# Performance work log

Hardware: AMD Instinct MI355X
Metric: run time of the kernel (lower is better)

The kernel has to match this reference:

```python
import jax, jax.numpy as jnp
import numpy as np

B, T, C, D = 8, 4096, 1024, 128  # batch, seq (=block_size), dim_embd, head_features

def setup_inputs() -> dict:
    key = jax.random.key(0)
    k1, k2, k3, k4 = jax.random.split(key, 4)
    s = 0.02
    return {
        "x": jax.random.normal(k1, (B, T, C), dtype=jnp.float32),
        "wq": jax.random.normal(k2, (C, D), dtype=jnp.float32) * s,
        "wk": jax.random.normal(k3, (C, D), dtype=jnp.float32) * s,
        "wv": jax.random.normal(k4, (C, D), dtype=jnp.float32) * s,
    }

def reference(x, wq, wk, wv):
    # q,k,v: [B,T,D]
    q = jnp.einsum('btc,cd->btd', x, wq)
    k = jnp.einsum('btc,cd->btd', x, wk)
    v = jnp.einsum('btc,cd->btd', x, wv)
    scale = k.shape[-1] ** -0.5
    wei = jnp.einsum('bqd,bkd->bqk', q, k) * scale  # [B,T,T]
    causal = jnp.tril(jnp.ones((T, T), dtype=bool))
    wei = jnp.where(causal, wei, -jnp.inf)
    attn = jax.nn.softmax(wei, axis=-1)  # dropout p=0.0 -> identity
    out = jnp.einsum('bqk,bkd->bqd', attn, v)  # [B,T,D]
    return out
```

## Files before the change

### kernel.cpp

```cpp
#include <hip/hip_runtime.h>

#define TT 4096
#define CC 1024
#define DD 128

typedef __attribute__((ext_vector_type(8))) short s16x8;
typedef __attribute__((ext_vector_type(4))) short s16x4;
typedef __attribute__((ext_vector_type(8))) __bf16 bf16x8;
typedef __attribute__((ext_vector_type(4))) float f32x4;

__device__ __forceinline__ short f2bf(float f) {
    union { float f; unsigned u; } v; v.f = f;
    unsigned r = v.u + 0x7fffu + ((v.u >> 16) & 1u);
    return (short)(r >> 16);
}

__device__ __forceinline__ unsigned cvt_pk(float lo, float hi) {
    unsigned r;
    asm("v_cvt_pk_bf16_f32 %0, %1, %2" : "=v"(r) : "v"(lo), "v"(hi));
    return r;
}

__device__ __forceinline__ f32x4 mfma16(s16x8 a, s16x8 b, f32x4 c) {
    return __builtin_amdgcn_mfma_f32_16x16x32_bf16(
        __builtin_bit_cast(bf16x8, a), __builtin_bit_cast(bf16x8, b), c, 0, 0, 0);
}

__device__ __forceinline__ void gload_lds16(const short* g, short* l) {
    __builtin_amdgcn_global_load_lds(
        (const __attribute__((address_space(1))) void*)g,
        (__attribute__((address_space(3))) void*)l, 16, 0, 0);
}

__global__ void wt_kernel(const float* __restrict__ wq, const float* __restrict__ wk,
                          const float* __restrict__ wv, short* __restrict__ wT) {
    int idx = blockIdx.x * 256 + threadIdx.x;
    int d = idx & 127;
    int c = (idx >> 7) & 1023;
    int wsel = idx >> 17;
    const float* w = (wsel == 0) ? wq : (wsel == 1) ? wk : wv;
    float v = w[(size_t)c * DD + d];
    if (wsel == 0) v *= 0.08838834764831845f;
    wT[(size_t)wsel * DD * CC + (size_t)d * CC + c] = f2bf(v);
}

__global__ __launch_bounds__(512)
void qkv_kernel(const float* __restrict__ x, const short* __restrict__ wT,
                short* __restrict__ qo, short* __restrict__ ko, short* __restrict__ vTo) {
    __shared__ short lw[2][384 * 64];
    const int mt = blockIdx.x;
    const int tid = threadIdx.x, lane = tid & 63, wid = tid >> 6;
    const int l15 = lane & 15, g = lane >> 4;
    const int wm = wid >> 1, wn = wid & 1;
    const int arow = mt * 128 + wm * 32 + l15;
    const float* xr0 = x + (size_t)arow * CC + g * 8;
    const float* xr1 = xr0 + (size_t)16 * CC;

    const f32x4 fz = {0.f, 0.f, 0.f, 0.f};
    f32x4 acc[2][12];
#pragma unroll
    for (int mr = 0; mr < 2; mr++)
#pragma unroll
        for (int nr = 0; nr < 12; nr++) acc[mr][nr] = fz;

    const int swr = wid * 48;
    const short* wsrc = wT + (size_t)(swr + (lane >> 3)) * CC + (lane & 7) * 8;

    float4 pa[2][2][2];
#define LOADA(kc) do { \
    _Pragma("unroll") for (int mr_ = 0; mr_ < 2; mr_++) \
    _Pragma("unroll") for (int ks_ = 0; ks_ < 2; ks_++) { \
        const float* p_ = (mr_ ? xr1 : xr0) + (kc) * 64 + ks_ * 32; \
        pa[mr_][ks_][0] = *(const float4*)p_; \
        pa[mr_][ks_][1] = *(const float4*)(p_ + 4); } \
} while (0)
#define STAGEW(kc, buf) do { \
    _Pragma("unroll") for (int j_ = 0; j_ < 6; j_++) \
        gload_lds16(wsrc + (size_t)(j_ * 8) * CC + (kc) * 64, &lw[buf][(swr + j_ * 8) * 64]); \
} while (0)

    LOADA(0);
    STAGEW(0, 0);
    asm volatile("s_waitcnt vmcnt(0)" ::: "memory");
    __builtin_amdgcn_s_barrier();
    int cur = 0;

    for (int kc = 0; kc < 16; kc++) {
        s16x8 af[2][2];
#pragma unroll
        for (int mr = 0; mr < 2; mr++)
#pragma unroll
            for (int ks = 0; ks < 2; ks++) {
                union { unsigned u[4]; s16x8 v; } cv;
                cv.u[0] = cvt_pk(pa[mr][ks][0].x, pa[mr][ks][0].y);
                cv.u[1] = cvt_pk(pa[mr][ks][0].z, pa[mr][ks][0].w);
                cv.u[2] = cvt_pk(pa[mr][ks][1].x, pa[mr][ks][1].y);
                cv.u[3] = cvt_pk(pa[mr][ks][1].z, pa[mr][ks][1].w);
                af[mr][ks] = cv.v;
            }
        if (kc < 15) { LOADA(kc + 1); STAGEW(kc + 1, cur ^ 1); }
        __builtin_amdgcn_s_setprio(1);
#pragma unroll
        for (int ks = 0; ks < 2; ks++)
#pragma unroll
            for (int nr = 0; nr < 12; nr++) {
                const s16x8 bfg = *(const s16x8*)
                    &lw[cur][(wn * 192 + nr * 16 + l15) * 64 + ks * 32 + g * 8];
                acc[0][nr] = mfma16(af[0][ks], bfg, acc[0][nr]);
                acc[1][nr] = mfma16(af[1][ks], bfg, acc[1][nr]);
            }
        __builtin_amdgcn_s_setprio(0);
        asm volatile("s_waitcnt vmcnt(0) lgkmcnt(0)" ::: "memory");
        __builtin_amdgcn_s_barrier();
        cur ^= 1;
    }

    const int bidx = mt >> 5;
    const int tb = (mt & 31) * 128 + wm * 32;
#pragma unroll
    for (int mr = 0; mr < 2; mr++)
#pragma unroll
        for (int nr = 0; nr < 12; nr++) {
            const int n = wn * 192 + nr * 16 + l15;
            if (n < 256) {
                short* dst; int d;
                if (n < 128) { dst = qo; d = n; } else { dst = ko; d = n - 128; }
#pragma unroll
                for (int i = 0; i < 4; i++) {
                    int t = tb + mr * 16 + g * 4 + i;
                    dst[((size_t)bidx * TT + t) * DD + d] = f2bf(acc[mr][nr][i]);
                }
            } else {
                const int d = n - 256;
                const int t = tb + mr * 16 + g * 4;
                uint2 u;
                u.x = cvt_pk(acc[mr][nr][0], acc[mr][nr][1]);
                u.y = cvt_pk(acc[mr][nr][2], acc[mr][nr][3]);
                *(uint2*)(vTo + ((size_t)bidx * DD + d) * TT + t) = u;
            }
        }
}

__device__ __forceinline__ void attn_stage(const short* kT, const short* vT, int kv0,
                                           short* lkb, short* lvb, int wid, int lane) {
#pragma unroll
    for (int j = 0; j < 4; j++) {
        int rbk = wid * 16 + j * 4;
        int rk = rbk + (lane >> 4);
        int ck = (lane & 15) ^ (rk & 7);
        gload_lds16(kT + (size_t)(kv0 + rk) * DD + ck * 8, lkb + rbk * 128);
        int rbv = wid * 32 + j * 8;
        int dv = rbv + (lane >> 3);
        int cv = (lane & 7) ^ (dv & 7);
        gload_lds16(vT + (size_t)dv * TT + kv0 + cv * 8, lvb + rbv * 64);
    }
}

__global__ __launch_bounds__(256)
void attn_kernel(const short* __restrict__ qb, const short* __restrict__ kb,
                 const short* __restrict__ vb, float* __restrict__ out,
                 float* __restrict__ opart, float2* __restrict__ mlpart) {
    const int qt = blockIdx.x;
    const int c  = blockIdx.y;
    const int b  = blockIdx.z;
    const int t0 = c * 16;
    if (t0 > qt) return;
    const int t1 = (t0 + 16 < qt + 1) ? t0 + 16 : qt + 1;
    const int nc = (qt >> 4) + 1;

    __shared__ short lk[2][64 * 128];
    __shared__ short lv[2][128 * 64];
    __shared__ short lp[4][1024];
    const int tid = threadIdx.x, lane = tid & 63, wid = tid >> 6;
    const int l15 = lane & 15, g = lane >> 4;
    const int wq0 = qt * 64 + wid * 16;
    const short* kT = kb + (size_t)b * TT * DD;
    const short* vT = vb + (size_t)b * DD * TT;
    char* lpw = (char*)&lp[wid][0];
    const f32x4 fz = {0.f, 0.f, 0.f, 0.f};

    s16x8 qf[4];
    {
        const short* qp = qb + ((size_t)b * TT + wq0 + l15) * DD + g * 8;
#pragma unroll
        for (int ks = 0; ks < 4; ks++) qf[ks] = *(const s16x8*)(qp + ks * 32);
    }
    f32x4 o[8];
#pragma unroll
    for (int n = 0; n < 8; n++) o[n] = fz;
    float rmax = -1e30f, rsum = 0.f;

    attn_stage(kT, vT, t0 * 64, lk[0], lv[0], wid, lane);
    asm volatile("s_waitcnt vmcnt(0)" ::: "memory");
    __builtin_amdgcn_s_barrier();
    int cur = 0;

    for (int t = t0; t < t1; t++) {
        if (t + 1 < t1) attn_stage(kT, vT, (t + 1) * 64, lk[cur ^ 1], lv[cur ^ 1], wid, lane);
        const int kv0 = t * 64;
        const char* lkc = (const char*)&lk[cur][0];
        const char* lvc = (const char*)&lv[cur][0];

        f32x4 s[4];
        __builtin_amdgcn_s_setprio(1);
#pragma unroll
        for (int sub = 0; sub < 4; sub++) {
            f32x4 a = fz;
#pragma unroll
            for (int ks = 0; ks < 4; ks++) {
                int row = sub * 16 + l15;
                int byte = (row * 256 + ks * 64 + g * 16) ^ ((row & 7) << 4);
                s16x8 kf = *(const s16x8*)(lkc + byte);
                a = mfma16(kf, qf[ks], a);
            }
            s[sub] = a;
        }
        __builtin_amdgcn_s_setprio(0);
        if (t == qt) {
#pragma unroll
            for (int sub = 0; sub < 4; sub++)
#pragma unroll
                for (int i = 0; i < 4; i++) {
                    int k = kv0 + sub * 16 + 4 * g + i;
                    if (k > wq0 + l15) s[sub][i] = -1e30f;
                }
        }
        float m0 = s[0][0];
#pragma unroll
        for (int sub = 0; sub < 4; sub++)
#pragma unroll
            for (int i = 0; i < 4; i++) m0 = fmaxf(m0, s[sub][i]);
        m0 = fmaxf(m0, __shfl_xor(m0, 16));
        m0 = fmaxf(m0, __shfl_xor(m0, 32));
        float mnew = fmaxf(rmax, m0);
        float scal = __expf(rmax - mnew);
        rmax = mnew;
        float ls = 0.f;
#pragma unroll
        for (int sub = 0; sub < 4; sub++)
#pragma unroll
            for (int i = 0; i < 4; i++) {
                float pv = __expf(s[sub][i] - mnew);
                s[sub][i] = pv;
                ls += pv;
            }
        ls += __shfl_xor(ls, 16);
        ls += __shfl_xor(ls, 32);
        rsum = rsum * scal + ls;
#pragma unroll
        for (int sub = 0; sub < 4; sub++) {
            uint2 w01;
            w01.x = cvt_pk(s[sub][0], s[sub][1]);
            w01.y = cvt_pk(s[sub][2], s[sub][3]);
            int byte = (l15 * 128 + sub * 32 + g * 8) ^ ((l15 & 7) << 4);
            *(uint2*)(lpw + byte) = w01;
        }
#pragma unroll
        for (int n = 0; n < 8; n++)
#pragma unroll
            for (int i = 0; i < 4; i++) o[n][i] *= scal;
        __builtin_amdgcn_s_setprio(1);
#pragma unroll
        for (int ks2 = 0; ks2 < 2; ks2++) {
            int pbyte = (l15 * 128 + ks2 * 64 + g * 16) ^ ((l15 & 7) << 4);
            s16x8 pf = *(const s16x8*)(lpw + pbyte);
#pragma unroll
            for (int n = 0; n < 8; n++) {
                int vrow = n * 16 + l15;
                int vbyte = (vrow * 128 + ks2 * 64 + g * 16) ^ ((vrow & 7) << 4);
                s16x8 vf = *(const s16x8*)(lvc + vbyte);
                o[n] = mfma16(vf, pf, o[n]);
            }
        }
        __builtin_amdgcn_s_setprio(0);
        asm volatile("s_waitcnt vmcnt(0) lgkmcnt(0)" ::: "memory");
        __builtin_amdgcn_s_barrier();
        cur ^= 1;
    }

    const int r = wid * 16 + l15;
    if (nc == 1) {
        float inv = 1.0f / rsum;
        float* orow = out + ((size_t)b * TT + qt * 64 + r) * DD;
#pragma unroll
        for (int n = 0; n < 8; n++) {
            float4 w;
            w.x = o[n][0] * inv; w.y = o[n][1] * inv;
            w.z = o[n][2] * inv; w.w = o[n][3] * inv;
            *(float4*)(orow + n * 16 + 4 * g) = w;
        }
    } else {
        const size_t pb = ((size_t)b * 48 + (qt - 16)) * 4 + c;
        float* prow = opart + pb * (64 * 128) + (size_t)r * 128;
#pragma unroll
        for (int n = 0; n < 8; n++) {
            float4 w;
            w.x = o[n][0]; w.y = o[n][1]; w.z = o[n][2]; w.w = o[n][3];
            *(float4*)(prow + n * 16 + 4 * g) = w;
        }
        if (g == 0) {
            float2 s2; s2.x = rmax; s2.y = rsum;
            mlpart[pb * 64 + r] = s2;
        }
    }
}

__global__ __launch_bounds__(256)
void comb_kernel(const float* __restrict__ opart, const float2* __restrict__ mlpart,
                 float* __restrict__ out) {
    const int qtm = blockIdx.x;
    const int b = blockIdx.y;
    const int qt = 16 + qtm;
    const int nc = (qt >> 4) + 1;
    const int tid = threadIdx.x;
    const int row = tid >> 2, quad = tid & 3;
    const size_t base = ((size_t)b * 48 + qtm) * 4;

    float M = -3e38f;
    for (int cc = 0; cc < nc; cc++)
        M = fmaxf(M, mlpart[(base + cc) * 64 + row].x);

    float acc[32];
#pragma unroll
    for (int k = 0; k < 32; k++) acc[k] = 0.f;
    float L = 0.f;
    for (int cc = 0; cc < nc; cc++) {
        float2 s = mlpart[(base + cc) * 64 + row];
        float wgt = __expf(s.x - M);
        L += wgt * s.y;
        const float* src = opart + (base + cc) * (64 * 128) + (size_t)row * 128 + quad * 32;
#pragma unroll
        for (int k = 0; k < 8; k++) {
            float4 v = *(const float4*)(src + k * 4);
            acc[k * 4 + 0] += wgt * v.x;
            acc[k * 4 + 1] += wgt * v.y;
            acc[k * 4 + 2] += wgt * v.z;
            acc[k * 4 + 3] += wgt * v.w;
        }
    }
    float inv = 1.0f / L;
    float* dst = out + ((size_t)b * TT + qt * 64 + row) * DD + quad * 32;
#pragma unroll
    for (int k = 0; k < 8; k++) {
        float4 w;
        w.x = acc[k * 4 + 0] * inv; w.y = acc[k * 4 + 1] * inv;
        w.z = acc[k * 4 + 2] * inv; w.w = acc[k * 4 + 3] * inv;
        *(float4*)(dst + k * 4) = w;
    }
}

extern "C" void kernel_launch(void* const* d_in, const int* in_sizes, int n_in,
                              void* d_out, int out_size, void* d_ws, size_t ws_size,
                              hipStream_t stream) {
    const float* x  = (const float*)d_in[0];
    const float* wq = (const float*)d_in[1];
    const float* wk = (const float*)d_in[2];
    const float* wv = (const float*)d_in[3];
    float* out = (float*)d_out;
    char* ws = (char*)d_ws;
    short* wT = (short*)ws;
    short* qb = (short*)(ws + 786432);
    short* kb = (short*)(ws + 786432 + 8388608);
    short* vb = (short*)(ws + 786432 + 16777216);
    float* opart = (float*)(ws + 786432 + 25165824);
    float2* mlpart = (float2*)(ws + 786432 + 25165824 + 50331648);

    wt_kernel<<<1536, 256, 0, stream>>>(wq, wk, wv, wT);
    qkv_kernel<<<256, 512, 0, stream>>>(x, wT, qb, kb, vb);
    attn_kernel<<<dim3(64, 4, 8), 256, 0, stream>>>(qb, kb, vb, out, opart, mlpart);
    comb_kernel<<<dim3(48, 8), 256, 0, stream>>>(opart, mlpart, out);
}
```

Measured before the change: 170.7 us.

## Double attention query tile to 128 rows with 8 waves sharing K/V loads

Each attention block now handles 128 query rows with 512 threads (8 waves) instead of 64 rows with 4 waves, so every K/V tile staged into LDS is reused by twice as many waves. Each wave now issues half as many staging loads, and waves whose query sub-tile ends before the diagonal skip compute on the final KV tile. The softmax scale is folded with log2(e) into Wq so exp2f replaces __expf. The split-KV partial buffers and the combine kernel are re-indexed for the new tiling. In exchange there are fewer blocks, idle waves on the diagonal tile, and higher per-block LDS and register pressure.

Result: slower. 220.8 us (+29.4%).

```diff
diff --git a/kernel.cpp b/kernel.cpp
--- a/kernel.cpp
+++ b/kernel.cpp
@@ -40,7 +40,7 @@
     int wsel = idx >> 17;
     const float* w = (wsel == 0) ? wq : (wsel == 1) ? wk : wv;
     float v = w[(size_t)c * DD + d];
-    if (wsel == 0) v *= 0.08838834764831845f;
+    if (wsel == 0) v *= 0.08838834764831845f * 1.4426950408889634f;
     wT[(size_t)wsel * DD * CC + (size_t)d * CC + c] = f2bf(v);
 }
 
@@ -141,39 +141,41 @@
         }
 }
 
-__device__ __forceinline__ void attn_stage(const short* kT, const short* vT, int kv0,
-                                           short* lkb, short* lvb, int wid, int lane) {
-#pragma unroll
-    for (int j = 0; j < 4; j++) {
-        int rbk = wid * 16 + j * 4;
+__device__ __forceinline__ void attn_stage8(const short* kT, const short* vT, int kv0,
+                                            short* lkb, short* lvb, int wid, int lane) {
+#pragma unroll
+    for (int j = 0; j < 2; j++) {
+        int rbk = wid * 8 + j * 4;
         int rk = rbk + (lane >> 4);
         int ck = (lane & 15) ^ (rk & 7);
         gload_lds16(kT + (size_t)(kv0 + rk) * DD + ck * 8, lkb + rbk * 128);
-        int rbv = wid * 32 + j * 8;
+        int rbv = wid * 16 + j * 8;
         int dv = rbv + (lane >> 3);
         int cv = (lane & 7) ^ (dv & 7);
         gload_lds16(vT + (size_t)dv * TT + kv0 + cv * 8, lvb + rbv * 64);
     }
 }
 
-__global__ __launch_bounds__(256)
+__global__ __launch_bounds__(512)
 void attn_kernel(const short* __restrict__ qb, const short* __restrict__ kb,
                  const short* __restrict__ vb, float* __restrict__ out,
                  float* __restrict__ opart, float2* __restrict__ mlpart) {
-    const int qt = blockIdx.x;
-    const int c  = blockIdx.y;
-    const int b  = blockIdx.z;
+    const int Q = blockIdx.x;
+    const int c = blockIdx.y;
+    const int b = blockIdx.z;
     const int t0 = c * 16;
-    if (t0 > qt) return;
-    const int t1 = (t0 + 16 < qt + 1) ? t0 + 16 : qt + 1;
-    const int nc = (qt >> 4) + 1;
+    const int tend = 2 * Q + 2;
+    if (t0 >= tend) return;
+    const int t1 = (t0 + 16 < tend) ? t0 + 16 : tend;
+    const int nc = (tend + 15) >> 4;
 
     __shared__ short lk[2][64 * 128];
     __shared__ short lv[2][128 * 64];
-    __shared__ short lp[4][1024];
+    __shared__ short lp[8][1024];
     const int tid = threadIdx.x, lane = tid & 63, wid = tid >> 6;
     const int l15 = lane & 15, g = lane >> 4;
-    const int wq0 = qt * 64 + wid * 16;
+    const int wq0 = Q * 128 + wid * 16;
+    const int tq_w = 2 * Q + (wid >> 2);
     const short* kT = kb + (size_t)b * TT * DD;
     const short* vT = vb + (size_t)b * DD * TT;
     char* lpw = (char*)&lp[wid][0];
@@ -190,89 +192,91 @@
     for (int n = 0; n < 8; n++) o[n] = fz;
     float rmax = -1e30f, rsum = 0.f;
 
-    attn_stage(kT, vT, t0 * 64, lk[0], lv[0], wid, lane);
+    attn_stage8(kT, vT, t0 * 64, lk[0], lv[0], wid, lane);
     asm volatile("s_waitcnt vmcnt(0)" ::: "memory");
     __builtin_amdgcn_s_barrier();
     int cur = 0;
 
     for (int t = t0; t < t1; t++) {
-        if (t + 1 < t1) attn_stage(kT, vT, (t + 1) * 64, lk[cur ^ 1], lv[cur ^ 1], wid, lane);
-        const int kv0 = t * 64;
-        const char* lkc = (const char*)&lk[cur][0];
-        const char* lvc = (const char*)&lv[cur][0];
-
-        f32x4 s[4];
-        __builtin_amdgcn_s_setprio(1);
-#pragma unroll
-        for (int sub = 0; sub < 4; sub++) {
-            f32x4 a = fz;
-#pragma unroll
-            for (int ks = 0; ks < 4; ks++) {
-                int row = sub * 16 + l15;
-                int byte = (row * 256 + ks * 64 + g * 16) ^ ((row & 7) << 4);
-                s16x8 kf = *(const s16x8*)(lkc + byte);
-                a = mfma16(kf, qf[ks], a);
-            }
-            s[sub] = a;
-        }
-        __builtin_amdgcn_s_setprio(0);
-        if (t == qt) {
+        if (t + 1 < t1) attn_stage8(kT, vT, (t + 1) * 64, lk[cur ^ 1], lv[cur ^ 1], wid, lane);
+        if (t <= tq_w) {
+            const int kv0 = t * 64;
+            const char* lkc = (const char*)&lk[cur][0];
+            const char* lvc = (const char*)&lv[cur][0];
+
+            f32x4 s[4];
+            __builtin_amdgcn_s_setprio(1);
+#pragma unroll
+            for (int sub = 0; sub < 4; sub++) {
+                f32x4 a = fz;
+#pragma unroll
+                for (int ks = 0; ks < 4; ks++) {
+                    int row = sub * 16 + l15;
+                    int byte = (row * 256 + ks * 64 + g * 16) ^ ((row & 7) << 4);
+                    s16x8 kf = *(const s16x8*)(lkc + byte);
+                    a = mfma16(kf, qf[ks], a);
+                }
+                s[sub] = a;
+            }
+            __builtin_amdgcn_s_setprio(0);
+            if (t == tq_w) {
+#pragma unroll
+                for (int sub = 0; sub < 4; sub++)
+#pragma unroll
+                    for (int i = 0; i < 4; i++) {
+                        int k = kv0 + sub * 16 + 4 * g + i;
+                        if (k > wq0 + l15) s[sub][i] = -1e30f;
+                    }
+            }
+            float m0 = s[0][0];
 #pragma unroll
             for (int sub = 0; sub < 4; sub++)
 #pragma unroll
+                for (int i = 0; i < 4; i++) m0 = fmaxf(m0, s[sub][i]);
+            m0 = fmaxf(m0, __shfl_xor(m0, 16));
+            m0 = fmaxf(m0, __shfl_xor(m0, 32));
+            float mnew = fmaxf(rmax, m0);
+            float scal = exp2f(rmax - mnew);
+            rmax = mnew;
+            float ls = 0.f;
+#pragma unroll
+            for (int sub = 0; sub < 4; sub++)
+#pragma unroll
                 for (int i = 0; i < 4; i++) {
-                    int k = kv0 + sub * 16 + 4 * g + i;
-                    if (k > wq0 + l15) s[sub][i] = -1e30f;
+                    float pv = exp2f(s[sub][i] - mnew);
+                    s[sub][i] = pv;
+                    ls += pv;
                 }
-        }
-        float m0 = s[0][0];
-#pragma unroll
-        for (int sub = 0; sub < 4; sub++)
-#pragma unroll
-            for (int i = 0; i < 4; i++) m0 = fmaxf(m0, s[sub][i]);
-        m0 = fmaxf(m0, __shfl_xor(m0, 16));
-        m0 = fmaxf(m0, __shfl_xor(m0, 32));
-        float mnew = fmaxf(rmax, m0);
-        float scal = __expf(rmax - mnew);
-        rmax = mnew;
-        float ls = 0.f;
-#pragma unroll
-        for (int sub = 0; sub < 4; sub++)
-#pragma unroll
-            for (int i = 0; i < 4; i++) {
-                float pv = __expf(s[sub][i] - mnew);
-                s[sub][i] = pv;
-                ls += pv;
-            }
-        ls += __shfl_xor(ls, 16);
-        ls += __shfl_xor(ls, 32);
-        rsum = rsum * scal + ls;
-#pragma unroll
-        for (int sub = 0; sub < 4; sub++) {
-            uint2 w01;
-            w01.x = cvt_pk(s[sub][0], s[sub][1]);
-            w01.y = cvt_pk(s[sub][2], s[sub][3]);
-            int byte = (l15 * 128 + sub * 32 + g * 8) ^ ((l15 & 7) << 4);
-            *(uint2*)(lpw + byte) = w01;
-        }
-#pragma unroll
-        for (int n = 0; n < 8; n++)
-#pragma unroll
-            for (int i = 0; i < 4; i++) o[n][i] *= scal;
-        __builtin_amdgcn_s_setprio(1);
-#pragma unroll
-        for (int ks2 = 0; ks2 < 2; ks2++) {
-            int pbyte = (l15 * 128 + ks2 * 64 + g * 16) ^ ((l15 & 7) << 4);
-            s16x8 pf = *(const s16x8*)(lpw + pbyte);
-#pragma unroll
-            for (int n = 0; n < 8; n++) {
-                int vrow = n * 16 + l15;
-                int vbyte = (vrow * 128 + ks2 * 64 + g * 16) ^ ((vrow & 7) << 4);
-                s16x8 vf = *(const s16x8*)(lvc + vbyte);
-                o[n] = mfma16(vf, pf, o[n]);
-            }
-        }
-        __builtin_amdgcn_s_setprio(0);
+            ls += __shfl_xor(ls, 16);
+            ls += __shfl_xor(ls, 32);
+            rsum = rsum * scal + ls;
+#pragma unroll
+            for (int sub = 0; sub < 4; sub++) {
+                uint2 w01;
+                w01.x = cvt_pk(s[sub][0], s[sub][1]);
+                w01.y = cvt_pk(s[sub][2], s[sub][3]);
+                int byte = (l15 * 128 + sub * 32 + g * 8) ^ ((l15 & 7) << 4);
+                *(uint2*)(lpw + byte) = w01;
+            }
+#pragma unroll
+            for (int n = 0; n < 8; n++)
+#pragma unroll
+                for (int i = 0; i < 4; i++) o[n][i] *= scal;
+            __builtin_amdgcn_s_setprio(1);
+#pragma unroll
+            for (int ks2 = 0; ks2 < 2; ks2++) {
+                int pbyte = (l15 * 128 + ks2 * 64 + g * 16) ^ ((l15 & 7) << 4);
+                s16x8 pf = *(const s16x8*)(lpw + pbyte);
+#pragma unroll
+                for (int n = 0; n < 8; n++) {
+                    int vrow = n * 16 + l15;
+                    int vbyte = (vrow * 128 + ks2 * 64 + g * 16) ^ ((vrow & 7) << 4);
+                    s16x8 vf = *(const s16x8*)(lvc + vbyte);
+                    o[n] = mfma16(vf, pf, o[n]);
+                }
+            }
+            __builtin_amdgcn_s_setprio(0);
+        }
         asm volatile("s_waitcnt vmcnt(0) lgkmcnt(0)" ::: "memory");
         __builtin_amdgcn_s_barrier();
         cur ^= 1;
@@ -281,7 +285,7 @@
     const int r = wid * 16 + l15;
     if (nc == 1) {
         float inv = 1.0f / rsum;
-        float* orow = out + ((size_t)b * TT + qt * 64 + r) * DD;
+        float* orow = out + ((size_t)b * TT + Q * 128 + r) * DD;
 #pragma unroll
         for (int n = 0; n < 8; n++) {
             float4 w;
@@ -290,8 +294,8 @@
             *(float4*)(orow + n * 16 + 4 * g) = w;
         }
     } else {
-        const size_t pb = ((size_t)b * 48 + (qt - 16)) * 4 + c;
-        float* prow = opart + pb * (64 * 128) + (size_t)r * 128;
+        const size_t pb = ((size_t)b * 24 + (Q - 8)) * 4 + c;
+        float* prow = opart + pb * (128 * 128) + (size_t)r * 128;
 #pragma unroll
         for (int n = 0; n < 8; n++) {
             float4 w;
@@ -300,7 +304,7 @@
         }
         if (g == 0) {
             float2 s2; s2.x = rmax; s2.y = rsum;
-            mlpart[pb * 64 + r] = s2;
+            mlpart[pb * 128 + r] = s2;
         }
     }
 }
@@ -308,27 +312,27 @@
 __global__ __launch_bounds__(256)
 void comb_kernel(const float* __restrict__ opart, const float2* __restrict__ mlpart,
                  float* __restrict__ out) {
-    const int qtm = blockIdx.x;
+    const int qh = blockIdx.x;
     const int b = blockIdx.y;
-    const int qt = 16 + qtm;
-    const int nc = (qt >> 4) + 1;
+    const int Q = 8 + (qh >> 1);
+    const int nc = (2 * Q + 2 + 15) >> 4;
     const int tid = threadIdx.x;
-    const int row = tid >> 2, quad = tid & 3;
-    const size_t base = ((size_t)b * 48 + qtm) * 4;
+    const int r = (qh & 1) * 64 + (tid >> 2), quad = tid & 3;
+    const size_t base = ((size_t)b * 24 + (Q - 8)) * 4;
 
     float M = -3e38f;
     for (int cc = 0; cc < nc; cc++)
-        M = fmaxf(M, mlpart[(base + cc) * 64 + row].x);
+        M = fmaxf(M, mlpart[(base + cc) * 128 + r].x);
 
     float acc[32];
 #pragma unroll
     for (int k = 0; k < 32; k++) acc[k] = 0.f;
     float L = 0.f;
     for (int cc = 0; cc < nc; cc++) {
-        float2 s = mlpart[(base + cc) * 64 + row];
-        float wgt = __expf(s.x - M);
+        float2 s = mlpart[(base + cc) * 128 + r];
+        float wgt = exp2f(s.x - M);
         L += wgt * s.y;
-        const float* src = opart + (base + cc) * (64 * 128) + (size_t)row * 128 + quad * 32;
+        const float* src = opart + (base + cc) * (128 * 128) + (size_t)r * 128 + quad * 32;
 #pragma unroll
         for (int k = 0; k < 8; k++) {
             float4 v = *(const float4*)(src + k * 4);
@@ -339,7 +343,7 @@
         }
     }
     float inv = 1.0f / L;
-    float* dst = out + ((size_t)b * TT + qt * 64 + row) * DD + quad * 32;
+    float* dst = out + ((size_t)b * TT + Q * 128 + r) * DD + quad * 32;
 #pragma unroll
     for (int k = 0; k < 8; k++) {
         float4 w;
@@ -367,6 +371,6 @@
 
     wt_kernel<<<1536, 256, 0, stream>>>(wq, wk, wv, wT);
     qkv_kernel<<<256, 512, 0, stream>>>(x, wT, qb, kb, vb);
-    attn_kernel<<<dim3(64, 4, 8), 256, 0, stream>>>(qb, kb, vb, out, opart, mlpart);
+    attn_kernel<<<dim3(32, 4, 8), 512, 0, stream>>>(qb, kb, vb, out, opart, mlpart);
     comb_kernel<<<dim3(48, 8), 256, 0, stream>>>(opart, mlpart, out);
 }
```
